# Kernel optimization log

Hardware: AMD Instinct MI355X
Metric: run time of the kernel (lower is better)

Reference implementation:

```python
import jax, jax.numpy as jnp
import numpy as np

# --- config (Qwen3-Next linear attention defaults) ---
B, S, H = 1, 256, 2048
NK, NV, DK, DV, K = 4, 32, 128, 128, 4
KEY_DIM = NK * DK          # 512
VAL_DIM = NV * DV          # 4096
CONV_DIM = 2 * KEY_DIM + VAL_DIM  # 5120
EPS = 1e-6


def setup_inputs() -> dict:
    key = jax.random.key(0)
    ks = jax.random.split(key, 8)
    rn = lambda k, shape, sc: jax.random.normal(k, shape, jnp.float32) * sc
    return {
        "hidden_states": jax.random.normal(ks[0], (B, S, H), jnp.float32),
        "w_qkvz": rn(ks[1], (2 * KEY_DIM + 2 * VAL_DIM, H), 0.02),  # in_proj_qkvz weight
        "w_ba": rn(ks[2], (2 * NV, H), 0.02),                        # in_proj_ba weight
        "w_out": rn(ks[3], (H, VAL_DIM), 0.02),                      # out_proj weight
        "conv_w": rn(ks[4], (CONV_DIM, 1, K), 0.1),                  # depthwise conv weight [C,1,K]
        "dt_bias": jnp.ones((NV,), jnp.float32),
        "A_log": jnp.zeros((NV,), jnp.float32),
        "norm_w": jnp.ones((DV,), jnp.float32),
    }


def reference(hidden_states, w_qkvz, w_ba, w_out, conv_w, dt_bias, A_log, norm_w):
    b, s, _ = hidden_states.shape
    # input projections (Linear without bias: x @ W.T)
    qkvz = hidden_states @ w_qkvz.T                      # [B,S,9216]
    ba = hidden_states @ w_ba.T                          # [B,S,64]
    q, k, v, z = jnp.split(qkvz, [KEY_DIM, 2 * KEY_DIM, 2 * KEY_DIM + VAL_DIM], axis=-1)
    beta, alpha = jnp.split(ba, 2, axis=-1)              # each [B,S,NV]

    # causal depthwise conv over concat(q,k,v), then silu
    qkv = jnp.concatenate([q, k, v], axis=-1).transpose(0, 2, 1)   # [B,C,S]
    qkv = jax.lax.conv_general_dilated(
        qkv, conv_w, window_strides=(1,), padding=[(K - 1, 0)],
        dimension_numbers=("NCH", "OIH", "NCH"), feature_group_count=CONV_DIM)
    qkv = jax.nn.silu(qkv).transpose(0, 2, 1)            # [B,S,C]
    q, k, v = jnp.split(qkv, [KEY_DIM, 2 * KEY_DIM], axis=-1)

    q = q.reshape(b, s, NK, DK)
    k = k.reshape(b, s, NK, DK)
    v = v.reshape(b, s, NV, DV)
    z = z.reshape(b, s, NV, DV)

    # GQA-style head expansion (repeat_interleave)
    ratio = NV // NK
    q = jnp.repeat(q, ratio, axis=2)                     # [B,S,NV,DK]
    k = jnp.repeat(k, ratio, axis=2)

    # NOTE: original computes g = -softplus(-A_log - alpha) but never uses it (dead code).
    beta_g = jax.nn.sigmoid(beta + dt_bias)[..., None]   # [B,S,NV,1]
    q = q * (DK ** -0.5)

    # naive delta-rule: full outer-product tensor + cumsum (memory-bound)
    kv = jnp.einsum("bsnk,bsnv->bsnkv", k, v * beta_g)   # [B,S,NV,DK,DV]
    out = jnp.einsum("bsnk,bsnkv->bsnv", q, jnp.cumsum(kv, axis=1))  # [B,S,NV,DV]

    # gated RMSNorm over head_v_dim in fp32
    of = out.astype(jnp.float32)
    var = jnp.mean(of * of, axis=-1, keepdims=True)
    of = of * jax.lax.rsqrt(var + EPS) * norm_w
    of = of * jax.nn.silu(z.astype(jnp.float32))

    return of.reshape(b, s, VAL_DIM) @ w_out.T           # [B,S,H]
```

## Files before the change

### kernel.cpp

```cpp
#include <hip/hip_runtime.h>
#include <hip/hip_bf16.h>

#define S_LEN   256
#define HID     2048
#define NVH     32
#define DKD     128
#define DVD     128
#define KEYDIM  512
#define VALDIM  4096
#define CONVDIM 5120
#define QKVZ_N  9216
#define EPS_F   1e-6f

typedef __attribute__((ext_vector_type(8))) short bf16x8;
typedef __attribute__((ext_vector_type(4))) float f32x4;

__device__ __forceinline__ unsigned short f2bf(float f) {
    union { float f; unsigned int i; } v; v.f = f;
    unsigned int x = v.i;
    return (unsigned short)((x + 0x7FFFu + ((x >> 16) & 1u)) >> 16);
}
__device__ __forceinline__ unsigned int pk2(float x, float y) {
    union { __hip_bfloat162 h; unsigned int u; } c;
    c.h = __float22bfloat162_rn(float2{x, y});
    return c.u;
}
__device__ __forceinline__ float4 asf4(uint4 u) {
    union { uint4 u; float4 f; } c; c.u = u; return c.f;
}
__device__ __forceinline__ uint4 cvt8_pack(float4 a, float4 b) {
    uint4 r;
    r.x = pk2(a.x, a.y); r.y = pk2(a.z, a.w);
    r.z = pk2(b.x, b.y); r.w = pk2(b.z, b.w);
    return r;
}

template<bool A_F32>
__global__ __launch_bounds__(256, 2)
void gemm_tile(const void* __restrict__ Ap, const float* __restrict__ B,
               float* __restrict__ Cpart, int N, int K, int kc) {
    __shared__ __align__(16) unsigned short As[128][72];
    __shared__ __align__(16) unsigned short Bs[128][72];

    const int tid  = threadIdx.x;
    const int lane = tid & 63, wave = tid >> 6;
    const int wm = wave >> 1, wn = wave & 1;
    const int quad = lane >> 4, l16 = lane & 15;
    const int m0 = blockIdx.y * 128, n0 = blockIdx.x * 128;
    const int kbeg = blockIdx.z * kc;
    const int niter = kc >> 6;

    const int lc = (tid & 7) << 3;
    const int lr = tid >> 3;

    f32x4 acc[4][4];
#pragma unroll
    for (int i = 0; i < 4; i++)
#pragma unroll
        for (int j = 0; j < 4; j++) acc[i][j] = (f32x4){0.f, 0.f, 0.f, 0.f};

    uint4 qa[8], qb[8];

    auto ld_tiles = [&](int kk) {
        if constexpr (A_F32) {
            const float* a = (const float*)Ap + (size_t)(m0 + lr) * K + kk + lc;
#pragma unroll
            for (int i = 0; i < 4; i++) {
                qa[2 * i]     = *(const uint4*)(a + (size_t)(32 * i) * K);
                qa[2 * i + 1] = *(const uint4*)(a + (size_t)(32 * i) * K + 4);
            }
        } else {
            const unsigned short* a = (const unsigned short*)Ap + (size_t)(m0 + lr) * K + kk + lc;
#pragma unroll
            for (int i = 0; i < 4; i++)
                qa[i] = *(const uint4*)(a + (size_t)(32 * i) * K);
        }
        const float* b = B + (size_t)(n0 + lr) * K + kk + lc;
#pragma unroll
        for (int i = 0; i < 4; i++) {
            qb[2 * i]     = *(const uint4*)(b + (size_t)(32 * i) * K);
            qb[2 * i + 1] = *(const uint4*)(b + (size_t)(32 * i) * K + 4);
        }
    };
    auto st_tiles = [&]() {
#pragma unroll
        for (int i = 0; i < 4; i++) {
            if constexpr (A_F32)
                *(uint4*)(&As[lr + 32 * i][lc]) = cvt8_pack(asf4(qa[2 * i]), asf4(qa[2 * i + 1]));
            else
                *(uint4*)(&As[lr + 32 * i][lc]) = qa[i];
            *(uint4*)(&Bs[lr + 32 * i][lc]) = cvt8_pack(asf4(qb[2 * i]), asf4(qb[2 * i + 1]));
        }
    };

    ld_tiles(kbeg);
    st_tiles();
    __syncthreads();

    for (int it = 0; it < niter; ++it) {
        if (it + 1 < niter) ld_tiles(kbeg + (it + 1) * 64);

        bf16x8 af[2][4], bfr[2][4];
#pragma unroll
        for (int t = 0; t < 4; t++) {
#pragma unroll
            for (int ks = 0; ks < 2; ks++) {
                af[ks][t]  = *(const bf16x8*)(&As[wm * 64 + t * 16 + l16][ks * 32 + quad * 8]);
                bfr[ks][t] = *(const bf16x8*)(&Bs[wn * 64 + t * 16 + l16][ks * 32 + quad * 8]);
            }
        }
#pragma unroll
        for (int ks = 0; ks < 2; ks++)
#pragma unroll
            for (int i = 0; i < 4; i++)
#pragma unroll
                for (int j = 0; j < 4; j++)
                    acc[i][j] = __builtin_amdgcn_mfma_f32_16x16x32_bf16(af[ks][i], bfr[ks][j], acc[i][j], 0, 0, 0);

        if (it + 1 < niter) {
            __syncthreads();
            st_tiles();
            __syncthreads();
        }
    }

    float* C = Cpart + (size_t)blockIdx.z * 256 * N;
#pragma unroll
    for (int i = 0; i < 4; i++)
#pragma unroll
        for (int j = 0; j < 4; j++)
#pragma unroll
            for (int r = 0; r < 4; r++) {
                int row = m0 + wm * 64 + i * 16 + quad * 4 + r;
                int col = n0 + wn * 64 + j * 16 + l16;
                C[(size_t)row * N + col] = acc[i][j][r];
            }
}

template<int P>
__global__ void reduce_sum(const float* __restrict__ part, float* __restrict__ out, int n) {
    int i = (blockIdx.x * 256 + threadIdx.x) * 4;
    if (i >= n) return;
    float4 s = *(const float4*)(part + i);
#pragma unroll
    for (int p = 1; p < P; p++) {
        float4 v = *(const float4*)(part + (size_t)p * n + i);
        s.x += v.x; s.y += v.y; s.z += v.z; s.w += v.w;
    }
    *(float4*)(out + i) = s;
}

__global__ __launch_bounds__(256)
void ba_proj(const float* __restrict__ hs,
             const float* __restrict__ w_ba,
             float* __restrict__ ba) {
    int s = blockIdx.x;
    int n = threadIdx.x & 63, seg = threadIdx.x >> 6;
    const float* x = hs + (size_t)s * HID + seg * 512;
    const float* w = w_ba + (size_t)n * HID + seg * 512;
    float acc = 0.f;
#pragma unroll 4
    for (int k = 0; k < 512; k += 4) {
        float4 xv = *(const float4*)(x + k);
        float4 wv = *(const float4*)(w + k);
        acc += xv.x * wv.x + xv.y * wv.y + xv.z * wv.z + xv.w * wv.w;
    }
    __shared__ float parts[4][64];
    parts[seg][n] = acc;
    __syncthreads();
    if (threadIdx.x < 64)
        ba[s * 64 + threadIdx.x] = parts[0][threadIdx.x] + parts[1][threadIdx.x]
                                 + parts[2][threadIdx.x] + parts[3][threadIdx.x];
}

__global__ void conv_silu(const float* __restrict__ qkvz,
                          const float* __restrict__ conv_w,
                          float* __restrict__ out) {
    int idx = blockIdx.x * blockDim.x + threadIdx.x;
    if (idx >= S_LEN * CONVDIM) return;
    int s = idx / CONVDIM, c = idx % CONVDIM;
    float acc = 0.f;
#pragma unroll
    for (int j = 0; j < 4; j++) {
        int t = s - 3 + j;
        if (t >= 0) acc += qkvz[(size_t)t * QKVZ_N + c] * conv_w[c * 4 + j];
    }
    out[idx] = acc / (1.f + __expf(-acc));
}

__global__ __launch_bounds__(256)
void scores_k(const float* __restrict__ conv, const float* __restrict__ ba,
              const float* __restrict__ dt_bias, float* __restrict__ scores) {
    if (blockIdx.x > blockIdx.y) return;
    int hk = blockIdx.z;
    int s0 = blockIdx.y * 16, t0 = blockIdx.x * 16;
    __shared__ float Qs[16][132], Ks[16][132];
    int tid = threadIdx.x;
    int qoff = hk * DKD;
    int koff = KEYDIM + hk * DKD;
    for (int idx = tid; idx < 16 * 128; idx += 256) {
        int i = idx >> 7, d = idx & 127;
        Qs[i][d] = conv[(size_t)(s0 + i) * CONVDIM + qoff + d];
        Ks[i][d] = conv[(size_t)(t0 + i) * CONVDIM + koff + d];
    }
    __syncthreads();
    int tx = tid & 15, ty = tid >> 4;
    int s = s0 + ty, t = t0 + tx;
    float dot = 0.f;
    for (int d = 0; d < 128; d++) dot += Qs[ty][d] * Ks[tx][d];
    float base = (t <= s) ? dot * 0.08838834764831845f : 0.f;
#pragma unroll
    for (int v = 0; v < 8; v++) {
        int n = hk * 8 + v;
        float b = ba[t * 64 + n] + dt_bias[n];
        float bg = 1.f / (1.f + __expf(-b));
        scores[((size_t)n * 256 + s) * 256 + t] = base * bg;
    }
}

__global__ __launch_bounds__(256)
void attn_v(const float* __restrict__ scores, const float* __restrict__ conv,
            float* __restrict__ attn) {
    int n = blockIdx.y, s0 = blockIdx.x * 16;
    int voff = 2 * KEYDIM + n * DVD;
    __shared__ float Ss[16][17];
    __shared__ float Vs[16][132];
    int tid = threadIdx.x, sy = tid >> 4, dx = tid & 15;
    float acc[8] = {0.f, 0.f, 0.f, 0.f, 0.f, 0.f, 0.f, 0.f};
    for (int t0 = 0; t0 <= s0; t0 += 16) {
        Ss[sy][dx] = scores[((size_t)n * 256 + s0 + sy) * 256 + t0 + dx];
        const float* vp = conv + (size_t)(t0 + sy) * CONVDIM + voff + dx * 8;
        *(float4*)&Vs[sy][dx * 8]     = *(const float4*)vp;
        *(float4*)&Vs[sy][dx * 8 + 4] = *(const float4*)(vp + 4);
        __syncthreads();
#pragma unroll
        for (int j = 0; j < 16; j++) {
            float sv = Ss[sy][j];
#pragma unroll
            for (int r = 0; r < 8; r++) acc[r] += sv * Vs[j][dx + 16 * r];
        }
        __syncthreads();
    }
    float* op = attn + ((size_t)(s0 + sy) * NVH + n) * DVD;
#pragma unroll
    for (int r = 0; r < 8; r++) op[dx + 16 * r] = acc[r];
}

__global__ __launch_bounds__(128)
void rmsnorm_gate(const float* __restrict__ attn, const float* __restrict__ qkvz,
                  const float* __restrict__ norm_w,
                  unsigned short* __restrict__ normed) {
    int s = blockIdx.x >> 5, n = blockIdx.x & 31;
    int d = threadIdx.x;
    float x = attn[((size_t)s * NVH + n) * DVD + d];
    float sq = x * x;
#pragma unroll
    for (int off = 32; off > 0; off >>= 1) sq += __shfl_down(sq, off, 64);
    __shared__ float parts[2];
    if ((d & 63) == 0) parts[d >> 6] = sq;
    __syncthreads();
    float ms = (parts[0] + parts[1]) * (1.f / 128.f);
    float inv = rsqrtf(ms + EPS_F);
    float z = qkvz[(size_t)s * QKVZ_N + CONVDIM + n * DVD + d];
    float sz = z / (1.f + __expf(-z));
    float v = x * inv * norm_w[d] * sz;
    normed[((size_t)s * NVH + n) * DVD + d] = f2bf(v);
}

extern "C" void kernel_launch(void* const* d_in, const int* in_sizes, int n_in,
                              void* d_out, int out_size, void* d_ws, size_t ws_size,
                              hipStream_t stream) {
    const float* hs      = (const float*)d_in[0];
    const float* w_qkvz  = (const float*)d_in[1];
    const float* w_ba    = (const float*)d_in[2];
    const float* w_out   = (const float*)d_in[3];
    const float* conv_w  = (const float*)d_in[4];
    const float* dt_bias = (const float*)d_in[5];
    const float* norm_w  = (const float*)d_in[7];

    char* ws = (char*)d_ws;
    float* qkvz = (float*)ws;  ws += (size_t)S_LEN * QKVZ_N * 4;
    float* ba   = (float*)ws;  ws += (size_t)S_LEN * 64 * 4;
    float* conv = (float*)ws;  ws += (size_t)S_LEN * CONVDIM * 4;
    char* regB = ws;
    float* scratch1 = (float*)regB;
    unsigned short* normed = (unsigned short*)regB;
    float* scratch2 = (float*)(regB + 2097152);
    float* attn   = (float*)(regB + 2097152);
    float* scores = (float*)(regB + 2097152 + 4194304);

    const bool big = ws_size >= (size_t)54 * 1024 * 1024;
    const int sk1 = big ? 4 : 2;
    const int sk2 = big ? 16 : 8;

    gemm_tile<true><<<dim3(QKVZ_N / 128, 2, sk1), 256, 0, stream>>>(hs, w_qkvz, scratch1, QKVZ_N, HID, HID / sk1);
    ba_proj<<<S_LEN, 256, 0, stream>>>(hs, w_ba, ba);
    if (big) reduce_sum<4><<<(S_LEN * QKVZ_N) / 1024, 256, 0, stream>>>(scratch1, qkvz, S_LEN * QKVZ_N);
    else     reduce_sum<2><<<(S_LEN * QKVZ_N) / 1024, 256, 0, stream>>>(scratch1, qkvz, S_LEN * QKVZ_N);
    conv_silu<<<(S_LEN * CONVDIM) / 256, 256, 0, stream>>>(qkvz, conv_w, conv);
    scores_k<<<dim3(16, 16, 4), 256, 0, stream>>>(conv, ba, dt_bias, scores);
    attn_v<<<dim3(16, NVH), 256, 0, stream>>>(scores, conv, attn);
    rmsnorm_gate<<<S_LEN * NVH, 128, 0, stream>>>(attn, qkvz, norm_w, normed);
    gemm_tile<false><<<dim3(HID / 128, 2, sk2), 256, 0, stream>>>(normed, w_out, scratch2, HID, VALDIM, VALDIM / sk2);
    if (big) reduce_sum<16><<<(S_LEN * HID) / 1024, 256, 0, stream>>>(scratch2, (float*)d_out, S_LEN * HID);
    else     reduce_sum<8><<<(S_LEN * HID) / 1024, 256, 0, stream>>>(scratch2, (float*)d_out, S_LEN * HID);
}
```

Before: 275.8 us.

## Double-buffer GEMM LDS tiles with XOR swizzle and 512-thread blocks

Reworks the split-K bf16 MFMA GEMM to use two LDS buffers, so the next tile is stored while the current one is computed, with one barrier per iteration instead of two. It replaces padded LDS rows with an XOR swizzle to avoid bank conflicts. Block size doubles to 8 waves, each holding a 64x32 sub-tile, which halves accumulator registers per thread. The risk is fewer MFMAs per LDS fragment load and higher LDS use per block, which could cut occupancy.

Measured after the change: 283.3 us. +2.7%, slower.

```diff
diff --git a/kernel.cpp b/kernel.cpp
--- a/kernel.cpp
+++ b/kernel.cpp
@@ -28,99 +28,112 @@
 __device__ __forceinline__ float4 asf4(uint4 u) {
     union { uint4 u; float4 f; } c; c.u = u; return c.f;
 }
-__device__ __forceinline__ uint4 cvt8_pack(float4 a, float4 b) {
-    uint4 r;
-    r.x = pk2(a.x, a.y); r.y = pk2(a.z, a.w);
-    r.z = pk2(b.x, b.y); r.w = pk2(b.z, b.w);
-    return r;
+__device__ __forceinline__ uint2 cvt4(float4 a) {
+    uint2 r; r.x = pk2(a.x, a.y); r.y = pk2(a.z, a.w); return r;
 }
 
 template<bool A_F32>
-__global__ __launch_bounds__(256, 2)
+__global__ __launch_bounds__(512, 2)
 void gemm_tile(const void* __restrict__ Ap, const float* __restrict__ B,
                float* __restrict__ Cpart, int N, int K, int kc) {
-    __shared__ __align__(16) unsigned short As[128][72];
-    __shared__ __align__(16) unsigned short Bs[128][72];
+    __shared__ __align__(16) unsigned short As[2][128][64];
+    __shared__ __align__(16) unsigned short Bs[2][128][64];
 
     const int tid  = threadIdx.x;
     const int lane = tid & 63, wave = tid >> 6;
-    const int wm = wave >> 1, wn = wave & 1;
+    const int wm = wave >> 2, wn = wave & 3;
     const int quad = lane >> 4, l16 = lane & 15;
     const int m0 = blockIdx.y * 128, n0 = blockIdx.x * 128;
     const int kbeg = blockIdx.z * kc;
     const int niter = kc >> 6;
 
-    const int lc = (tid & 7) << 3;
-    const int lr = tid >> 3;
-
-    f32x4 acc[4][4];
+    const int rF = tid >> 4;
+    const int cF = (tid & 15) * 4;
+    const int rH = tid >> 3;
+    const int cH = (tid & 7) * 8;
+
+    f32x4 acc[4][2];
 #pragma unroll
     for (int i = 0; i < 4; i++)
 #pragma unroll
-        for (int j = 0; j < 4; j++) acc[i][j] = (f32x4){0.f, 0.f, 0.f, 0.f};
-
-    uint4 qa[8], qb[8];
+        for (int j = 0; j < 2; j++) acc[i][j] = (f32x4){0.f, 0.f, 0.f, 0.f};
+
+    uint4 qa[4], qb[4];
 
     auto ld_tiles = [&](int kk) {
         if constexpr (A_F32) {
-            const float* a = (const float*)Ap + (size_t)(m0 + lr) * K + kk + lc;
-#pragma unroll
-            for (int i = 0; i < 4; i++) {
-                qa[2 * i]     = *(const uint4*)(a + (size_t)(32 * i) * K);
-                qa[2 * i + 1] = *(const uint4*)(a + (size_t)(32 * i) * K + 4);
-            }
-        } else {
-            const unsigned short* a = (const unsigned short*)Ap + (size_t)(m0 + lr) * K + kk + lc;
+            const float* a = (const float*)Ap + (size_t)(m0 + rF) * K + kk + cF;
 #pragma unroll
             for (int i = 0; i < 4; i++)
                 qa[i] = *(const uint4*)(a + (size_t)(32 * i) * K);
-        }
-        const float* b = B + (size_t)(n0 + lr) * K + kk + lc;
+        } else {
+            const unsigned short* a = (const unsigned short*)Ap + (size_t)(m0 + rH) * K + kk + cH;
+#pragma unroll
+            for (int i = 0; i < 2; i++)
+                qa[i] = *(const uint4*)(a + (size_t)(64 * i) * K);
+        }
+        const float* b = B + (size_t)(n0 + rF) * K + kk + cF;
+#pragma unroll
+        for (int i = 0; i < 4; i++)
+            qb[i] = *(const uint4*)(b + (size_t)(32 * i) * K);
+    };
+
+    auto st_tiles = [&](int buf) {
+        if constexpr (A_F32) {
+#pragma unroll
+            for (int i = 0; i < 4; i++) {
+                int r = rF + 32 * i;
+                int col = ((((tid & 15) >> 1) ^ (r & 7)) << 3) + (tid & 1) * 4;
+                *(uint2*)(&As[buf][r][col]) = cvt4(asf4(qa[i]));
+            }
+        } else {
+#pragma unroll
+            for (int i = 0; i < 2; i++) {
+                int r = rH + 64 * i;
+                int col = ((tid & 7) ^ (r & 7)) << 3;
+                *(uint4*)(&As[buf][r][col]) = qa[i];
+            }
+        }
 #pragma unroll
         for (int i = 0; i < 4; i++) {
-            qb[2 * i]     = *(const uint4*)(b + (size_t)(32 * i) * K);
-            qb[2 * i + 1] = *(const uint4*)(b + (size_t)(32 * i) * K + 4);
+            int r = rF + 32 * i;
+            int col = ((((tid & 15) >> 1) ^ (r & 7)) << 3) + (tid & 1) * 4;
+            *(uint2*)(&Bs[buf][r][col]) = cvt4(asf4(qb[i]));
         }
     };
-    auto st_tiles = [&]() {
-#pragma unroll
-        for (int i = 0; i < 4; i++) {
-            if constexpr (A_F32)
-                *(uint4*)(&As[lr + 32 * i][lc]) = cvt8_pack(asf4(qa[2 * i]), asf4(qa[2 * i + 1]));
-            else
-                *(uint4*)(&As[lr + 32 * i][lc]) = qa[i];
-            *(uint4*)(&Bs[lr + 32 * i][lc]) = cvt8_pack(asf4(qb[2 * i]), asf4(qb[2 * i + 1]));
+
+    auto compute = [&](int buf) {
+#pragma unroll
+        for (int ks = 0; ks < 2; ks++) {
+            bf16x8 af[4], bfr[2];
+#pragma unroll
+            for (int i = 0; i < 4; i++) {
+                int r = wm * 64 + i * 16 + l16;
+                af[i] = *(const bf16x8*)(&As[buf][r][(((ks << 2) | quad) ^ (l16 & 7)) << 3]);
+            }
+#pragma unroll
+            for (int j = 0; j < 2; j++) {
+                int r = wn * 32 + j * 16 + l16;
+                bfr[j] = *(const bf16x8*)(&Bs[buf][r][(((ks << 2) | quad) ^ (l16 & 7)) << 3]);
+            }
+#pragma unroll
+            for (int i = 0; i < 4; i++)
+#pragma unroll
+                for (int j = 0; j < 2; j++)
+                    acc[i][j] = __builtin_amdgcn_mfma_f32_16x16x32_bf16(af[i], bfr[j], acc[i][j], 0, 0, 0);
         }
     };
 
     ld_tiles(kbeg);
-    st_tiles();
+    st_tiles(0);
     __syncthreads();
 
     for (int it = 0; it < niter; ++it) {
         if (it + 1 < niter) ld_tiles(kbeg + (it + 1) * 64);
-
-        bf16x8 af[2][4], bfr[2][4];
-#pragma unroll
-        for (int t = 0; t < 4; t++) {
-#pragma unroll
-            for (int ks = 0; ks < 2; ks++) {
-                af[ks][t]  = *(const bf16x8*)(&As[wm * 64 + t * 16 + l16][ks * 32 + quad * 8]);
-                bfr[ks][t] = *(const bf16x8*)(&Bs[wn * 64 + t * 16 + l16][ks * 32 + quad * 8]);
-            }
-        }
-#pragma unroll
-        for (int ks = 0; ks < 2; ks++)
-#pragma unroll
-            for (int i = 0; i < 4; i++)
-#pragma unroll
-                for (int j = 0; j < 4; j++)
-                    acc[i][j] = __builtin_amdgcn_mfma_f32_16x16x32_bf16(af[ks][i], bfr[ks][j], acc[i][j], 0, 0, 0);
-
+        compute(it & 1);
         if (it + 1 < niter) {
+            st_tiles((it + 1) & 1);
             __syncthreads();
-            st_tiles();
-            __syncthreads();
         }
     }
 
@@ -128,11 +141,11 @@
 #pragma unroll
     for (int i = 0; i < 4; i++)
 #pragma unroll
-        for (int j = 0; j < 4; j++)
+        for (int j = 0; j < 2; j++)
 #pragma unroll
             for (int r = 0; r < 4; r++) {
                 int row = m0 + wm * 64 + i * 16 + quad * 4 + r;
-                int col = n0 + wn * 64 + j * 16 + l16;
+                int col = n0 + wn * 32 + j * 16 + l16;
                 C[(size_t)row * N + col] = acc[i][j][r];
             }
 }
@@ -293,7 +306,7 @@
     const int sk1 = big ? 4 : 2;
     const int sk2 = big ? 16 : 8;
 
-    gemm_tile<true><<<dim3(QKVZ_N / 128, 2, sk1), 256, 0, stream>>>(hs, w_qkvz, scratch1, QKVZ_N, HID, HID / sk1);
+    gemm_tile<true><<<dim3(QKVZ_N / 128, 2, sk1), 512, 0, stream>>>(hs, w_qkvz, scratch1, QKVZ_N, HID, HID / sk1);
     ba_proj<<<S_LEN, 256, 0, stream>>>(hs, w_ba, ba);
     if (big) reduce_sum<4><<<(S_LEN * QKVZ_N) / 1024, 256, 0, stream>>>(scratch1, qkvz, S_LEN * QKVZ_N);
     else     reduce_sum<2><<<(S_LEN * QKVZ_N) / 1024, 256, 0, stream>>>(scratch1, qkvz, S_LEN * QKVZ_N);
@@ -301,7 +314,7 @@
     scores_k<<<dim3(16, 16, 4), 256, 0, stream>>>(conv, ba, dt_bias, scores);
     attn_v<<<dim3(16, NVH), 256, 0, stream>>>(scores, conv, attn);
     rmsnorm_gate<<<S_LEN * NVH, 128, 0, stream>>>(attn, qkvz, norm_w, normed);
-    gemm_tile<false><<<dim3(HID / 128, 2, sk2), 256, 0, stream>>>(normed, w_out, scratch2, HID, VALDIM, VALDIM / sk2);
+    gemm_tile<false><<<dim3(HID / 128, 2, sk2), 512, 0, stream>>>(normed, w_out, scratch2, HID, VALDIM, VALDIM / sk2);
     if (big) reduce_sum<16><<<(S_LEN * HID) / 1024, 256, 0, stream>>>(scratch2, (float*)d_out, S_LEN * HID);
     else     reduce_sum<8><<<(S_LEN * HID) / 1024, 256, 0, stream>>>(scratch2, (float*)d_out, S_LEN * HID);
 }
```

## Replace GEMM tiles with full-M LDS-direct-load kernel and pre-converted bf16 activations

Applied to the files above, without the earlier changes.

Pre-converts hidden_states to bf16 in a separate kernel. Both projection GEMMs move to a new kernel where each block covers all 256 rows and a narrow N slice. That kernel loads A (bf16) and B (fp32 weights) straight into LDS with global_load_lds and an XOR swizzle, and converts B to bf16 in registers. The aim is to remove the register round-trip and repeated conversion in the old tile loader, and to read each weight tile once instead of once per M-block. The costs are an extra kernel launch, fp32 weights kept in LDS, a single-buffered stage/compute loop, and a changed split-K for the output projection.

Result: faster. 256.6 us (-7.0%).

```diff
diff --git a/kernel.cpp b/kernel.cpp
--- a/kernel.cpp
+++ b/kernel.cpp
@@ -25,116 +25,121 @@
     c.h = __float22bfloat162_rn(float2{x, y});
     return c.u;
 }
-__device__ __forceinline__ float4 asf4(uint4 u) {
-    union { uint4 u; float4 f; } c; c.u = u; return c.f;
-}
-__device__ __forceinline__ uint4 cvt8_pack(float4 a, float4 b) {
+__device__ __forceinline__ bf16x8 pack_bf8(float4 lo, float4 hi) {
+    union { uint4 u; bf16x8 h; } c;
+    c.u.x = pk2(lo.x, lo.y); c.u.y = pk2(lo.z, lo.w);
+    c.u.z = pk2(hi.x, hi.y); c.u.w = pk2(hi.z, hi.w);
+    return c.h;
+}
+__device__ __forceinline__ void gl_lds16(const void* g, void* l) {
+    __builtin_amdgcn_global_load_lds(
+        (const __attribute__((address_space(1))) unsigned int*)g,
+        (__attribute__((address_space(3))) unsigned int*)l,
+        16, 0, 0);
+}
+
+template<int NT>
+__global__ __launch_bounds__(256, 3)
+void gemm_sn(const unsigned short* __restrict__ A, const float* __restrict__ B,
+             float* __restrict__ Cpart, int N, int K, int kc) {
+    __shared__ __align__(16) unsigned short As[256][64];
+    __shared__ __align__(16) float Bs[NT][64];
+
+    const int tid  = threadIdx.x;
+    const int lane = tid & 63, wave = tid >> 6;
+    const int quad = lane >> 4, l16 = lane & 15;
+    const int n0 = blockIdx.x * NT;
+    const int kbeg = blockIdx.y * kc;
+    const int niter = kc >> 6;
+    constexpr int NB = NT / 16;
+
+    const int a_ro = lane >> 3;
+    const int a_gc = (lane & 7) ^ a_ro;
+    const int b_ro = lane >> 4;
+    const int b_cs = lane & 15;
+
+    f32x4 acc[4][NB];
+#pragma unroll
+    for (int i = 0; i < 4; i++)
+#pragma unroll
+        for (int j = 0; j < NB; j++) acc[i][j] = (f32x4){0.f, 0.f, 0.f, 0.f};
+
+    auto stage = [&](int kk) {
+#pragma unroll
+        for (int t = 0; t < 8; ++t) {
+            int rbase = wave * 64 + t * 8;
+            gl_lds16(A + (size_t)(rbase + a_ro) * K + kk + a_gc * 8,
+                     &As[rbase][0]);
+        }
+#pragma unroll
+        for (int t = 0; t < NT / 16; ++t) {
+            int rbase = wave * (NT / 4) + t * 4;
+            int r = rbase + b_ro;
+            int gc = b_cs ^ (r & 7);
+            gl_lds16(B + (size_t)(n0 + r) * K + kk + gc * 4,
+                     &Bs[rbase][0]);
+        }
+    };
+
+    auto compute = [&]() {
+#pragma unroll
+        for (int ks = 0; ks < 2; ++ks) {
+            bf16x8 af[4];
+#pragma unroll
+            for (int i = 0; i < 4; ++i) {
+                int r = wave * 64 + i * 16 + l16;
+                int c = (ks * 4 + quad) ^ (l16 & 7);
+                af[i] = *(const bf16x8*)(&As[r][c * 8]);
+            }
+#pragma unroll
+            for (int j = 0; j < NB; ++j) {
+                int r = j * 16 + l16;
+                int x = l16 & 7;
+                int c0 = (ks * 8 + quad * 2) ^ x;
+                int c1 = (ks * 8 + quad * 2 + 1) ^ x;
+                float4 lo = *(const float4*)(&Bs[r][c0 * 4]);
+                float4 hi = *(const float4*)(&Bs[r][c1 * 4]);
+                bf16x8 bfr = pack_bf8(lo, hi);
+#pragma unroll
+                for (int i = 0; i < 4; ++i)
+                    acc[i][j] = __builtin_amdgcn_mfma_f32_16x16x32_bf16(af[i], bfr, acc[i][j], 0, 0, 0);
+            }
+        }
+    };
+
+    stage(kbeg);
+    for (int it = 0; it < niter; ++it) {
+        __syncthreads();
+        compute();
+        if (it + 1 < niter) {
+            __syncthreads();
+            stage(kbeg + (it + 1) * 64);
+        }
+    }
+
+    float* C = Cpart + (size_t)blockIdx.y * 256 * N;
+#pragma unroll
+    for (int i = 0; i < 4; i++)
+#pragma unroll
+        for (int j = 0; j < NB; j++)
+#pragma unroll
+            for (int r = 0; r < 4; r++) {
+                int row = wave * 64 + i * 16 + quad * 4 + r;
+                int col = n0 + j * 16 + l16;
+                C[(size_t)row * N + col] = acc[i][j][r];
+            }
+}
+
+__global__ __launch_bounds__(256)
+void cvt_bf16(const float* __restrict__ in, unsigned short* __restrict__ out, int n8) {
+    int i = blockIdx.x * 256 + threadIdx.x;
+    if (i >= n8) return;
+    const float4* p = (const float4*)in + (size_t)i * 2;
+    float4 a = p[0], b = p[1];
     uint4 r;
     r.x = pk2(a.x, a.y); r.y = pk2(a.z, a.w);
     r.z = pk2(b.x, b.y); r.w = pk2(b.z, b.w);
-    return r;
-}
-
-template<bool A_F32>
-__global__ __launch_bounds__(256, 2)
-void gemm_tile(const void* __restrict__ Ap, const float* __restrict__ B,
-               float* __restrict__ Cpart, int N, int K, int kc) {
-    __shared__ __align__(16) unsigned short As[128][72];
-    __shared__ __align__(16) unsigned short Bs[128][72];
-
-    const int tid  = threadIdx.x;
-    const int lane = tid & 63, wave = tid >> 6;
-    const int wm = wave >> 1, wn = wave & 1;
-    const int quad = lane >> 4, l16 = lane & 15;
-    const int m0 = blockIdx.y * 128, n0 = blockIdx.x * 128;
-    const int kbeg = blockIdx.z * kc;
-    const int niter = kc >> 6;
-
-    const int lc = (tid & 7) << 3;
-    const int lr = tid >> 3;
-
-    f32x4 acc[4][4];
-#pragma unroll
-    for (int i = 0; i < 4; i++)
-#pragma unroll
-        for (int j = 0; j < 4; j++) acc[i][j] = (f32x4){0.f, 0.f, 0.f, 0.f};
-
-    uint4 qa[8], qb[8];
-
-    auto ld_tiles = [&](int kk) {
-        if constexpr (A_F32) {
-            const float* a = (const float*)Ap + (size_t)(m0 + lr) * K + kk + lc;
-#pragma unroll
-            for (int i = 0; i < 4; i++) {
-                qa[2 * i]     = *(const uint4*)(a + (size_t)(32 * i) * K);
-                qa[2 * i + 1] = *(const uint4*)(a + (size_t)(32 * i) * K + 4);
-            }
-        } else {
-            const unsigned short* a = (const unsigned short*)Ap + (size_t)(m0 + lr) * K + kk + lc;
-#pragma unroll
-            for (int i = 0; i < 4; i++)
-                qa[i] = *(const uint4*)(a + (size_t)(32 * i) * K);
-        }
-        const float* b = B + (size_t)(n0 + lr) * K + kk + lc;
-#pragma unroll
-        for (int i = 0; i < 4; i++) {
-            qb[2 * i]     = *(const uint4*)(b + (size_t)(32 * i) * K);
-            qb[2 * i + 1] = *(const uint4*)(b + (size_t)(32 * i) * K + 4);
-        }
-    };
-    auto st_tiles = [&]() {
-#pragma unroll
-        for (int i = 0; i < 4; i++) {
-            if constexpr (A_F32)
-                *(uint4*)(&As[lr + 32 * i][lc]) = cvt8_pack(asf4(qa[2 * i]), asf4(qa[2 * i + 1]));
-            else
-                *(uint4*)(&As[lr + 32 * i][lc]) = qa[i];
-            *(uint4*)(&Bs[lr + 32 * i][lc]) = cvt8_pack(asf4(qb[2 * i]), asf4(qb[2 * i + 1]));
-        }
-    };
-
-    ld_tiles(kbeg);
-    st_tiles();
-    __syncthreads();
-
-    for (int it = 0; it < niter; ++it) {
-        if (it + 1 < niter) ld_tiles(kbeg + (it + 1) * 64);
-
-        bf16x8 af[2][4], bfr[2][4];
-#pragma unroll
-        for (int t = 0; t < 4; t++) {
-#pragma unroll
-            for (int ks = 0; ks < 2; ks++) {
-                af[ks][t]  = *(const bf16x8*)(&As[wm * 64 + t * 16 + l16][ks * 32 + quad * 8]);
-                bfr[ks][t] = *(const bf16x8*)(&Bs[wn * 64 + t * 16 + l16][ks * 32 + quad * 8]);
-            }
-        }
-#pragma unroll
-        for (int ks = 0; ks < 2; ks++)
-#pragma unroll
-            for (int i = 0; i < 4; i++)
-#pragma unroll
-                for (int j = 0; j < 4; j++)
-                    acc[i][j] = __builtin_amdgcn_mfma_f32_16x16x32_bf16(af[ks][i], bfr[ks][j], acc[i][j], 0, 0, 0);
-
-        if (it + 1 < niter) {
-            __syncthreads();
-            st_tiles();
-            __syncthreads();
-        }
-    }
-
-    float* C = Cpart + (size_t)blockIdx.z * 256 * N;
-#pragma unroll
-    for (int i = 0; i < 4; i++)
-#pragma unroll
-        for (int j = 0; j < 4; j++)
-#pragma unroll
-            for (int r = 0; r < 4; r++) {
-                int row = m0 + wm * 64 + i * 16 + quad * 4 + r;
-                int col = n0 + wn * 64 + j * 16 + l16;
-                C[(size_t)row * N + col] = acc[i][j][r];
-            }
+    *((uint4*)out + i) = r;
 }
 
 template<int P>
@@ -282,6 +287,8 @@
     float* qkvz = (float*)ws;  ws += (size_t)S_LEN * QKVZ_N * 4;
     float* ba   = (float*)ws;  ws += (size_t)S_LEN * 64 * 4;
     float* conv = (float*)ws;  ws += (size_t)S_LEN * CONVDIM * 4;
+    unsigned short* abf = (unsigned short*)ws;
+    ws += (size_t)S_LEN * HID * 2;
     char* regB = ws;
     float* scratch1 = (float*)regB;
     unsigned short* normed = (unsigned short*)regB;
@@ -289,11 +296,12 @@
     float* attn   = (float*)(regB + 2097152);
     float* scores = (float*)(regB + 2097152 + 4194304);
 
-    const bool big = ws_size >= (size_t)54 * 1024 * 1024;
+    const bool big = ws_size >= (size_t)55 * 1024 * 1024;
     const int sk1 = big ? 4 : 2;
-    const int sk2 = big ? 16 : 8;
-
-    gemm_tile<true><<<dim3(QKVZ_N / 128, 2, sk1), 256, 0, stream>>>(hs, w_qkvz, scratch1, QKVZ_N, HID, HID / sk1);
+
+    cvt_bf16<<<(S_LEN * HID / 8) / 256, 256, 0, stream>>>(hs, abf, S_LEN * HID / 8);
+    if (big) gemm_sn<64><<<dim3(QKVZ_N / 64, 4), 256, 0, stream>>>(abf, w_qkvz, scratch1, QKVZ_N, HID, HID / 4);
+    else     gemm_sn<64><<<dim3(QKVZ_N / 64, 2), 256, 0, stream>>>(abf, w_qkvz, scratch1, QKVZ_N, HID, HID / 2);
     ba_proj<<<S_LEN, 256, 0, stream>>>(hs, w_ba, ba);
     if (big) reduce_sum<4><<<(S_LEN * QKVZ_N) / 1024, 256, 0, stream>>>(scratch1, qkvz, S_LEN * QKVZ_N);
     else     reduce_sum<2><<<(S_LEN * QKVZ_N) / 1024, 256, 0, stream>>>(scratch1, qkvz, S_LEN * QKVZ_N);
@@ -301,7 +309,6 @@
     scores_k<<<dim3(16, 16, 4), 256, 0, stream>>>(conv, ba, dt_bias, scores);
     attn_v<<<dim3(16, NVH), 256, 0, stream>>>(scores, conv, attn);
     rmsnorm_gate<<<S_LEN * NVH, 128, 0, stream>>>(attn, qkvz, norm_w, normed);
-    gemm_tile<false><<<dim3(HID / 128, 2, sk2), 256, 0, stream>>>(normed, w_out, scratch2, HID, VALDIM, VALDIM / sk2);
-    if (big) reduce_sum<16><<<(S_LEN * HID) / 1024, 256, 0, stream>>>(scratch2, (float*)d_out, S_LEN * HID);
-    else     reduce_sum<8><<<(S_LEN * HID) / 1024, 256, 0, stream>>>(scratch2, (float*)d_out, S_LEN * HID);
-}
+    gemm_sn<32><<<dim3(HID / 32, 8), 256, 0, stream>>>(normed, w_out, scratch2, HID, VALDIM, VALDIM / 8);
+    reduce_sum<8><<<(S_LEN * HID) / 1024, 256, 0, stream>>>(scratch2, (float*)d_out, S_LEN * HID);
+}
```
